# Performance work log

Measured on AMD Instinct MI355X. Metric: run time of the kernel, lower is better.

## Reference

```python
import jax, jax.numpy as jnp
import numpy as np

E, S, G, H, O = 50000, 16, 64, 256, 16


def _mlp(x, W0, b0, W1, b1, W2, b2):
    # x: [..., 2] -> [..., out]
    x = jax.nn.relu(x @ W0 + b0)
    x = jax.nn.relu(x @ W1 + b1)
    return x @ W2 + b2


def setup_inputs() -> dict:
    key = jax.random.key(0)
    ks = jax.random.split(key, 9)
    ob = jax.random.normal(ks[0], (E, S, 3), dtype=jnp.float32)
    action = jax.random.randint(ks[1], (E, S), 0, O).astype(jnp.int64)
    graph_ids = jnp.sort(jax.random.randint(ks[2], (E,), 0, G)).astype(jnp.int32)
    def lin(k, fin, fout):
        return jax.random.normal(k, (fin, fout), dtype=jnp.float32) / jnp.sqrt(jnp.float32(fin))
    return {
        "ob": ob, "action": action, "graph_ids": graph_ids,
        "aW0": lin(ks[3], 2, H), "ab0": jnp.zeros((H,), jnp.float32),
        "aW1": lin(ks[4], H, H), "ab1": jnp.zeros((H,), jnp.float32),
        "aW2": lin(ks[5], H, O), "ab2": jnp.zeros((O,), jnp.float32),
        "cW0": lin(ks[6], 2, H), "cb0": jnp.zeros((H,), jnp.float32),
        "cW1": lin(ks[7], H, H), "cb1": jnp.zeros((H,), jnp.float32),
        "cW2": lin(ks[8], H, 1), "cb2": jnp.zeros((1,), jnp.float32),
    }


def reference(ob, action, graph_ids, aW0, ab0, aW1, ab1, aW2, ab2,
              cW0, cb0, cW1, cb1, cW2, cb2):
    num_edges = ob.shape[0]
    # edge_mask: torch `ob.select(2,0).long() == 0` (truncation toward zero)
    edge_mask = ob[..., 0].astype(jnp.int32) == 0            # [E,S] bool
    mf = edge_mask.astype(ob.dtype)                          # [E,S]
    h = ob[..., 1:3]                                         # [E,S,2]

    # Actor logits over all (edge,sample); mask replaces gather/scatter
    logits = _mlp(h, aW0, ab0, aW1, ab1, aW2, ab2)           # [E,S,O]
    logp = jax.nn.log_softmax(logits, axis=-1)               # [E,S,O]

    # log-prob of given actions, scattered to zeros outside the mask
    alp = jnp.take_along_axis(logp, action[..., None], axis=-1)[..., 0]
    action_log_probs = alp * mf                              # [E,S]

    # critic edge values, scattered to zeros outside the mask
    vals = _mlp(h, cW0, cb0, cW1, cb1, cW2, cb2)[..., 0] * mf  # [E,S]

    # entropy averaged over masked (subgraph) entries only
    ent = -jnp.sum(jnp.exp(logp) * logp, axis=-1)            # [E,S]
    avg_entropy = jnp.sum(ent * mf) / jnp.sum(mf)

    # sum_efeat: per-graph segment sum over edges, divided by num_edges
    value_preds = jax.ops.segment_sum(vals, graph_ids, num_segments=G) / num_edges  # [G,S]

    return action_log_probs, avg_entropy, value_preds, edge_mask
```

## Files before the change

### kernel.cpp

```cpp
#include <hip/hip_runtime.h>
#include <stdint.h>


typedef __attribute__((ext_vector_type(8))) short bf16x8;
typedef __attribute__((ext_vector_type(4))) float f32x4;
typedef __attribute__((ext_vector_type(4))) uint32_t u32x4;

#define NROWS    800000
#define NCHUNK   12500
#define OUT_ENT  800000
#define OUT_VP   800001
#define OUT_MASK 801025

#define SWZ(row) ((((row) & 7) << 4) ^ (((row) & 16) << 1))

__device__ __forceinline__ short f2bf(float x) {
  union { float f; uint32_t u; } v; v.f = x;
  return (short)(uint16_t)((v.u + 0x7FFFu + ((v.u >> 16) & 1u)) >> 16);
}
__device__ __forceinline__ float bf2f(short h) {
  union { uint32_t u; float f; } v; v.u = ((uint32_t)(uint16_t)h) << 16;
  return v.f;
}
template <int C>
__device__ __forceinline__ float dppf(float x) {
  int r = __builtin_amdgcn_update_dpp(0, __builtin_bit_cast(int, x), C, 0xF, 0xF, true);
  return __builtin_bit_cast(float, r);
}
__device__ __forceinline__ float red16_sum(float x) {
  x += dppf<0xB1>(x); x += dppf<0x4E>(x); x += dppf<0x124>(x); x += dppf<0x128>(x); return x;
}
__device__ __forceinline__ float red16_max(float x) {
  x = fmaxf(x, dppf<0xB1>(x)); x = fmaxf(x, dppf<0x4E>(x));
  x = fmaxf(x, dppf<0x124>(x)); x = fmaxf(x, dppf<0x128>(x)); return x;
}
__device__ __forceinline__ uint32_t cvt_pk_bf16(float a, float b) {
  uint32_t r; asm("v_cvt_pk_bf16_f32 %0, %1, %2" : "=v"(r) : "v"(a), "v"(b)); return r;
}

__global__ void zero_kernel(float* out, float* wsf) {
  int t = threadIdx.x + blockIdx.x * blockDim.x;
  for (int i = t; i < 1025; i += 1024) out[OUT_ENT + i] = 0.0f;
  if (t == 0) { wsf[0] = 0.0f; wsf[1] = 0.0f; }
}
__global__ void final_kernel(float* out, const float* wsf) {
  if (threadIdx.x == 0 && blockIdx.x == 0)
    out[OUT_ENT] = (wsf[1] > 0.0f) ? (wsf[0] / wsf[1]) : 0.0f;
}

#define L_ACT1 0
#define L_ACT2 32768
#define L_W2H  65536
#define L_W0   73728
#define L_B0   75776
#define L_OB   76800
#define L_SZ   78848

__global__ void __launch_bounds__(512, 2) ac_main(
    const float* __restrict__ ob, const int* __restrict__ action,
    const int* __restrict__ graph_ids,
    const float* __restrict__ aW0, const float* __restrict__ ab0,
    const float* __restrict__ aW1, const float* __restrict__ ab1,
    const float* __restrict__ aW2, const float* __restrict__ ab2,
    const float* __restrict__ cW0, const float* __restrict__ cb0,
    const float* __restrict__ cW1, const float* __restrict__ cb1,
    const float* __restrict__ cW2, const float* __restrict__ cb2,
    float* __restrict__ out, float* __restrict__ wsf)
{
  extern __shared__ char smem[];
  float* w0buf = (float*)(smem + L_W0);
  float* b0buf = (float*)(smem + L_B0);
  float* obufA = (float*)(smem + L_OB);
  float* vbuf  = (float*)(smem + L_ACT2);
  const f32x4* w04 = (const f32x4*)(smem + L_W0);
  const f32x4* b04 = (const f32x4*)(smem + L_B0);
  __shared__ float went[8], wmf[8];

  const int b = blockIdx.x;
  const int role = (b >> 8) & 1;
  const int pid  = (b & 255) | ((b >> 9) << 8);
  const int stride = 512;

  const int tid = threadIdx.x, lane = tid & 63, wave = tid >> 6;
  const int l15 = lane & 15, l4 = lane >> 4;

  const float* W0s = role ? cW0 : aW0;
  const float* B0s = role ? cb0 : ab0;
  const float* W1s = role ? cW1 : aW1;
  const float* B1s = role ? cb1 : ab1;

  w0buf[tid] = W0s[tid];
  if (tid < 256) b0buf[tid] = B0s[tid];
  if (!role) {
    for (int id = tid; id < 4096; id += 512) {
      int n = id >> 8, k = id & 255;
      *(short*)(smem + L_W2H + n * 512 + ((k * 2) ^ SWZ(n))) = f2bf(aW2[k * 16 + n]);
    }
  }
  const int colbase = wave * 32;
  float b1lane[2] = { B1s[colbase + l15], B1s[colbase + 16 + l15] };
  float b2lane = 0.0f, w2c0 = 0.0f, w2c1 = 0.0f, cb2v = 0.0f;
  if (!role) b2lane = ab2[l15];
  else { w2c0 = cW2[colbase + l15]; w2c1 = cW2[colbase + 16 + l15]; cb2v = cb2[0]; }

  bf16x8 bh[2][8];
  #pragma unroll
  for (int ct = 0; ct < 2; ++ct) {
    const int n = colbase + ct * 16 + l15;
    #pragma unroll
    for (int ks = 0; ks < 8; ++ks) {
      const int k0 = ks * 32 + 8 * l4;
      bf16x8 h8;
      #pragma unroll
      for (int j = 0; j < 8; ++j) h8[j] = f2bf(W1s[(k0 + j) * 256 + n]);
      bh[ct][ks] = h8;
    }
  }
  float sob = 0.0f;
  if (tid < 192) { obufA[tid] = ob[pid * 192 + tid]; }
  { int cn = pid + stride; if (cn < NCHUNK && tid < 192) sob = ob[cn * 192 + tid]; }
  __syncthreads();

  float entacc = 0.0f, mfacc = 0.0f;
  int buf = 0;
  for (int c = pid; c < NCHUNK; c += stride, buf ^= 1) {
    const int row0 = c * 64;
    const float* ocur = obufA + buf * 256;
    float* onxt = (float*)(obufA + (buf ^ 1) * 256);

    if (!role && tid < 64)
      out[OUT_MASK + row0 + tid] = ((int)ocur[tid * 3] == 0) ? 1.0f : 0.0f;
    {
      const int kb = tid & 31;
      f32x4 wa0 = w04[kb * 2], wa1 = w04[kb * 2 + 1];
      f32x4 wb0 = w04[64 + kb * 2], wb1 = w04[64 + kb * 2 + 1];
      f32x4 ba0 = b04[kb * 2], ba1 = b04[kb * 2 + 1];
      #pragma unroll
      for (int i = 0; i < 4; ++i) {
        int row = wave * 2 + 16 * i + (lane >> 5);
        float h0 = ocur[row * 3 + 1], h1 = ocur[row * 3 + 2];
        f32x4 va, vb;
        #pragma unroll
        for (int j = 0; j < 4; ++j) {
          va[j] = fmaxf(fmaf(h0, wa0[j], fmaf(h1, wb0[j], ba0[j])), 0.0f);
          vb[j] = fmaxf(fmaf(h0, wa1[j], fmaf(h1, wb1[j], ba1[j])), 0.0f);
        }
        u32x4 v;
        v[0] = cvt_pk_bf16(va[0], va[1]);
        v[1] = cvt_pk_bf16(va[2], va[3]);
        v[2] = cvt_pk_bf16(vb[0], vb[1]);
        v[3] = cvt_pk_bf16(vb[2], vb[3]);
        *(u32x4*)(smem + L_ACT1 + row * 512 + ((kb * 16) ^ SWZ(row))) = v;
      }
    }
    if (tid < 192) onxt[tid] = sob;
    { int c2 = c + 2 * stride; if (c2 < NCHUNK && tid < 192) sob = ob[c2 * 192 + tid]; }
    __syncthreads();

    float o0w0 = 0.0f;
    if (role && wave == 0) o0w0 = ocur[lane * 3];

    const bool evn = (l15 & 1) == 0;
    #pragma unroll 1
    for (int rtp = 0; rtp < 2; ++rtp) {
      f32x4 acc[2][2];
      #pragma unroll
      for (int h = 0; h < 2; ++h)
        #pragma unroll
        for (int ct = 0; ct < 2; ++ct)
          acc[h][ct] = (f32x4){b1lane[ct], b1lane[ct], b1lane[ct], b1lane[ct]};
      const int rA0 = rtp * 32 + l15, rA1 = rA0 + 16;
      #pragma unroll
      for (int ks = 0; ks < 8; ++ks) {
        const int cb = ks * 64 + 16 * l4;
        bf16x8 a0 = *(const bf16x8*)(smem + L_ACT1 + rA0 * 512 + (cb ^ SWZ(rA0)));
        bf16x8 a1 = *(const bf16x8*)(smem + L_ACT1 + rA1 * 512 + (cb ^ SWZ(rA1)));
        acc[0][0] = __builtin_amdgcn_mfma_f32_16x16x32_bf16(a0, bh[0][ks], acc[0][0], 0, 0, 0);
        acc[0][1] = __builtin_amdgcn_mfma_f32_16x16x32_bf16(a0, bh[1][ks], acc[0][1], 0, 0, 0);
        acc[1][0] = __builtin_amdgcn_mfma_f32_16x16x32_bf16(a1, bh[0][ks], acc[1][0], 0, 0, 0);
        acc[1][1] = __builtin_amdgcn_mfma_f32_16x16x32_bf16(a1, bh[1][ks], acc[1][1], 0, 0, 0);
      }
      if (!role) {
        #pragma unroll
        for (int ct = 0; ct < 2; ++ct) {
          const int colb = (colbase + ct * 16 + (l15 & ~1)) * 2;
          #pragma unroll
          for (int r = 0; r < 4; ++r) {
            float v0 = fmaxf(acc[0][ct][r], 0.0f);
            float v1 = fmaxf(acc[1][ct][r], 0.0f);
            float n0 = dppf<0xB1>(v0), n1 = dppf<0xB1>(v1);
            uint32_t w = cvt_pk_bf16(evn ? v0 : n1, evn ? n0 : v1);
            int rr = rtp * 32 + (evn ? 0 : 16) + 4 * l4 + r;
            *(uint32_t*)(smem + L_ACT2 + rr * 512 + (colb ^ SWZ(rr))) = w;
          }
        }
      } else {
        #pragma unroll
        for (int h = 0; h < 2; ++h) {
          #pragma unroll
          for (int r = 0; r < 4; ++r) {
            float p = fmaxf(acc[h][0][r], 0.0f) * w2c0
                    + fmaxf(acc[h][1][r], 0.0f) * w2c1;
            p = red16_sum(p);
            if (l15 == 0) vbuf[wave * 64 + rtp * 32 + h * 16 + 4 * l4 + r] = p;
          }
        }
      }
    }
    __syncthreads();

    if (!role) {
      const int rt = wave & 3, half = wave >> 2;
      const int rowA = rt * 16 + l15;
      const int swA = SWZ(rowA), swW = SWZ(l15);
      f32x4 ae = {b2lane, b2lane, b2lane, b2lane}, ao = {0.f,0.f,0.f,0.f};
      #pragma unroll
      for (int ks = 0; ks < 8; ks += 2) {
        const int cb0 = ks * 64 + 16 * l4, cb1 = cb0 + 64;
        bf16x8 a0 = *(const bf16x8*)(smem + L_ACT2 + rowA * 512 + (cb0 ^ swA));
        bf16x8 a1 = *(const bf16x8*)(smem + L_ACT2 + rowA * 512 + (cb1 ^ swA));
        bf16x8 w0f = *(const bf16x8*)(smem + L_W2H + l15 * 512 + (cb0 ^ swW));
        bf16x8 w1f = *(const bf16x8*)(smem + L_W2H + l15 * 512 + (cb1 ^ swW));
        ae = __builtin_amdgcn_mfma_f32_16x16x32_bf16(a0, w0f, ae, 0, 0, 0);
        ao = __builtin_amdgcn_mfma_f32_16x16x32_bf16(a1, w1f, ao, 0, 0, 0);
      }
      #pragma unroll
      for (int r2 = 0; r2 < 2; ++r2) {
        const int r = half * 2 + r2;
        const int rl = rt * 16 + 4 * l4 + r;
        float x = ae[r] + ao[r];
        float m = red16_max(x);
        float e = __expf(x - m);
        float s = red16_sum(e);
        float t = red16_sum(e * (x - m));
        float ls = __logf(s);
        float mfr = ((int)ob[(row0 + rl) * 3] == 0) ? 1.0f : 0.0f;
        int av = action[row0 + rl];
        if (l15 == av) out[row0 + rl] = (x - m - ls) * mfr;
        if (l15 == 0) { entacc += (ls - t / s) * mfr; mfacc += mfr; }
      }
    } else {
      if (wave == 0) {
        float v = 0.0f;
        #pragma unroll
        for (int w = 0; w < 8; ++w) v += vbuf[w * 64 + lane];
        if ((int)o0w0 == 0) {
          int g = graph_ids[c * 4 + (lane >> 4)];
          atomicAdd(&out[OUT_VP + g * 16 + (lane & 15)], (v + cb2v) * (1.0f / 50000.0f));
        }
      }
    }
  }
  if (!role) {
    #pragma unroll
    for (int d = 1; d < 64; d <<= 1) { entacc += __shfl_xor(entacc, d); mfacc += __shfl_xor(mfacc, d); }
    if (lane == 0) { went[wave] = entacc; wmf[wave] = mfacc; }
    __syncthreads();
    if (tid == 0) {
      float e = 0.f, m = 0.f;
      #pragma unroll
      for (int i = 0; i < 8; ++i) { e += went[i]; m += wmf[i]; }
      atomicAdd(&wsf[0], e); atomicAdd(&wsf[1], m);
    }
  }
}

extern "C" void kernel_launch(void* const* d_in, const int* in_sizes, int n_in,
                              void* d_out, int out_size, void* d_ws, size_t ws_size,
                              hipStream_t stream) {
  const float* ob     = (const float*)d_in[0];
  const int*   action = (const int*)d_in[1];
  const int*   gids   = (const int*)d_in[2];
  const float* aW0 = (const float*)d_in[3],  *ab0 = (const float*)d_in[4];
  const float* aW1 = (const float*)d_in[5],  *ab1 = (const float*)d_in[6];
  const float* aW2 = (const float*)d_in[7],  *ab2 = (const float*)d_in[8];
  const float* cW0 = (const float*)d_in[9],  *cb0 = (const float*)d_in[10];
  const float* cW1 = (const float*)d_in[11], *cb1 = (const float*)d_in[12];
  const float* cW2 = (const float*)d_in[13], *cb2 = (const float*)d_in[14];
  float* out = (float*)d_out;
  float* wsf = (float*)d_ws;

  zero_kernel<<<2, 512, 0, stream>>>(out, wsf);
  ac_main<<<1024, 512, L_SZ, stream>>>(ob, action, gids, aW0, ab0, aW1, ab1, aW2, ab2,
                                       cW0, cb0, cW1, cb1, cW2, cb2, out, wsf);
  final_kernel<<<1, 64, 0, stream>>>(out, wsf);
}
```

Baseline: 479.5 us.

## Compute layer-0 via MFMA and transpose layer-1 MFMA operands for direct stores

Layer 0 (K=2) is now computed with a bf16 MFMA using register-resident W0 fragments and bias-initialized accumulators, replacing the scalar FMA loop and its LDS weight buffers. The layer-1 MFMA swaps its A/B operands so each lane holds four consecutive columns of one row. That lets ACT2 be written with packed 8-byte stores instead of DPP lane swaps, and lets the critic dot product be reduced with two cross-lane shuffles. Mask values are read from the LDS ob buffer instead of global memory. The layer-0 MFMA wastes most of its K dimension and rounds the inputs h to bf16, a small extra precision loss.

```diff
diff --git a/kernel.cpp b/kernel.cpp
--- a/kernel.cpp
+++ b/kernel.cpp
@@ -4,6 +4,7 @@
 
 typedef __attribute__((ext_vector_type(8))) short bf16x8;
 typedef __attribute__((ext_vector_type(4))) float f32x4;
+typedef __attribute__((ext_vector_type(2))) uint32_t u32x2;
 typedef __attribute__((ext_vector_type(4))) uint32_t u32x4;
 
 #define NROWS    800000
@@ -18,10 +19,6 @@
   union { float f; uint32_t u; } v; v.f = x;
   return (short)(uint16_t)((v.u + 0x7FFFu + ((v.u >> 16) & 1u)) >> 16);
 }
-__device__ __forceinline__ float bf2f(short h) {
-  union { uint32_t u; float f; } v; v.u = ((uint32_t)(uint16_t)h) << 16;
-  return v.f;
-}
 template <int C>
 __device__ __forceinline__ float dppf(float x) {
   int r = __builtin_amdgcn_update_dpp(0, __builtin_bit_cast(int, x), C, 0xF, 0xF, true);
@@ -37,6 +34,9 @@
 __device__ __forceinline__ uint32_t cvt_pk_bf16(float a, float b) {
   uint32_t r; asm("v_cvt_pk_bf16_f32 %0, %1, %2" : "=v"(r) : "v"(a), "v"(b)); return r;
 }
+__device__ __forceinline__ bf16x8 frag_u32(uint32_t a, uint32_t b, uint32_t c, uint32_t d) {
+  union { u32x4 u; bf16x8 h; } v; v.u = (u32x4){a, b, c, d}; return v.h;
+}
 
 __global__ void zero_kernel(float* out, float* wsf) {
   int t = threadIdx.x + blockIdx.x * blockDim.x;
@@ -51,10 +51,8 @@
 #define L_ACT1 0
 #define L_ACT2 32768
 #define L_W2H  65536
-#define L_W0   73728
-#define L_B0   75776
-#define L_OB   76800
-#define L_SZ   78848
+#define L_OB   73728
+#define L_SZ   75776
 
 __global__ void __launch_bounds__(512, 2) ac_main(
     const float* __restrict__ ob, const int* __restrict__ action,
@@ -68,12 +66,8 @@
     float* __restrict__ out, float* __restrict__ wsf)
 {
   extern __shared__ char smem[];
-  float* w0buf = (float*)(smem + L_W0);
-  float* b0buf = (float*)(smem + L_B0);
   float* obufA = (float*)(smem + L_OB);
   float* vbuf  = (float*)(smem + L_ACT2);
-  const f32x4* w04 = (const f32x4*)(smem + L_W0);
-  const f32x4* b04 = (const f32x4*)(smem + L_B0);
   __shared__ float went[8], wmf[8];
 
   const int b = blockIdx.x;
@@ -89,19 +83,34 @@
   const float* W1s = role ? cW1 : aW1;
   const float* B1s = role ? cb1 : ab1;
 
-  w0buf[tid] = W0s[tid];
-  if (tid < 256) b0buf[tid] = B0s[tid];
+  const int colbase = wave * 32;
+
+  bf16x8 w0f[2];
+  #pragma unroll
+  for (int ct = 0; ct < 2; ++ct) {
+    int coln = colbase + ct * 16 + l15;
+    uint32_t p = 0u;
+    if (l4 == 0) p = cvt_pk_bf16(W0s[coln], W0s[256 + coln]);
+    w0f[ct] = frag_u32(p, 0u, 0u, 0u);
+  }
+  f32x4 b0i[2], b1i[2], w2r[2];
+  #pragma unroll
+  for (int ct = 0; ct < 2; ++ct)
+    #pragma unroll
+    for (int r = 0; r < 4; ++r) {
+      int idx = colbase + ct * 16 + 4 * l4 + r;
+      b0i[ct][r] = B0s[idx];
+      b1i[ct][r] = B1s[idx];
+      w2r[ct][r] = role ? cW2[idx] : 0.0f;
+    }
+  float b2lane = 0.0f, cb2v = 0.0f;
   if (!role) {
+    b2lane = ab2[l15];
     for (int id = tid; id < 4096; id += 512) {
       int n = id >> 8, k = id & 255;
       *(short*)(smem + L_W2H + n * 512 + ((k * 2) ^ SWZ(n))) = f2bf(aW2[k * 16 + n]);
     }
-  }
-  const int colbase = wave * 32;
-  float b1lane[2] = { B1s[colbase + l15], B1s[colbase + 16 + l15] };
-  float b2lane = 0.0f, w2c0 = 0.0f, w2c1 = 0.0f, cb2v = 0.0f;
-  if (!role) b2lane = ab2[l15];
-  else { w2c0 = cW2[colbase + l15]; w2c1 = cW2[colbase + 16 + l15]; cb2v = cb2[0]; }
+  } else cb2v = cb2[0];
 
   bf16x8 bh[2][8];
   #pragma unroll
@@ -130,111 +139,109 @@
 
     if (!role && tid < 64)
       out[OUT_MASK + row0 + tid] = ((int)ocur[tid * 3] == 0) ? 1.0f : 0.0f;
-    {
-      const int kb = tid & 31;
-      f32x4 wa0 = w04[kb * 2], wa1 = w04[kb * 2 + 1];
-      f32x4 wb0 = w04[64 + kb * 2], wb1 = w04[64 + kb * 2 + 1];
-      f32x4 ba0 = b04[kb * 2], ba1 = b04[kb * 2 + 1];
-      #pragma unroll
-      for (int i = 0; i < 4; ++i) {
-        int row = wave * 2 + 16 * i + (lane >> 5);
-        float h0 = ocur[row * 3 + 1], h1 = ocur[row * 3 + 2];
-        f32x4 va, vb;
-        #pragma unroll
-        for (int j = 0; j < 4; ++j) {
-          va[j] = fmaxf(fmaf(h0, wa0[j], fmaf(h1, wb0[j], ba0[j])), 0.0f);
-          vb[j] = fmaxf(fmaf(h0, wa1[j], fmaf(h1, wb1[j], ba1[j])), 0.0f);
-        }
-        u32x4 v;
-        v[0] = cvt_pk_bf16(va[0], va[1]);
-        v[1] = cvt_pk_bf16(va[2], va[3]);
-        v[2] = cvt_pk_bf16(vb[0], vb[1]);
-        v[3] = cvt_pk_bf16(vb[2], vb[3]);
-        *(u32x4*)(smem + L_ACT1 + row * 512 + ((kb * 16) ^ SWZ(row))) = v;
+    #pragma unroll
+    for (int rt = 0; rt < 4; ++rt) {
+      const int rowr = rt * 16 + l15;
+      float h0 = ocur[rowr * 3 + 1], h1 = ocur[rowr * 3 + 2];
+      uint32_t hp = (l4 == 0) ? cvt_pk_bf16(h0, h1) : 0u;
+      bf16x8 hf = frag_u32(hp, 0u, 0u, 0u);
+      #pragma unroll
+      for (int ct = 0; ct < 2; ++ct) {
+        f32x4 a = __builtin_amdgcn_mfma_f32_16x16x32_bf16(w0f[ct], hf, b0i[ct], 0, 0, 0);
+        u32x2 w;
+        w[0] = cvt_pk_bf16(fmaxf(a[0], 0.0f), fmaxf(a[1], 0.0f));
+        w[1] = cvt_pk_bf16(fmaxf(a[2], 0.0f), fmaxf(a[3], 0.0f));
+        *(u32x2*)(smem + L_ACT1 + rowr * 512 +
+                  ((colbase * 2 + ct * 32 + 8 * l4) ^ SWZ(rowr))) = w;
       }
     }
     if (tid < 192) onxt[tid] = sob;
     { int c2 = c + 2 * stride; if (c2 < NCHUNK && tid < 192) sob = ob[c2 * 192 + tid]; }
     __syncthreads();
 
-    float o0w0 = 0.0f;
-    if (role && wave == 0) o0w0 = ocur[lane * 3];
-
-    const bool evn = (l15 & 1) == 0;
     #pragma unroll 1
     for (int rtp = 0; rtp < 2; ++rtp) {
       f32x4 acc[2][2];
       #pragma unroll
-      for (int h = 0; h < 2; ++h)
-        #pragma unroll
-        for (int ct = 0; ct < 2; ++ct)
-          acc[h][ct] = (f32x4){b1lane[ct], b1lane[ct], b1lane[ct], b1lane[ct]};
-      const int rA0 = rtp * 32 + l15, rA1 = rA0 + 16;
+      for (int rt = 0; rt < 2; ++rt)
+        #pragma unroll
+        for (int ct = 0; ct < 2; ++ct) acc[rt][ct] = b1i[ct];
+      const int rB0 = rtp * 32 + l15, rB1 = rB0 + 16;
       #pragma unroll
       for (int ks = 0; ks < 8; ++ks) {
         const int cb = ks * 64 + 16 * l4;
-        bf16x8 a0 = *(const bf16x8*)(smem + L_ACT1 + rA0 * 512 + (cb ^ SWZ(rA0)));
-        bf16x8 a1 = *(const bf16x8*)(smem + L_ACT1 + rA1 * 512 + (cb ^ SWZ(rA1)));
-        acc[0][0] = __builtin_amdgcn_mfma_f32_16x16x32_bf16(a0, bh[0][ks], acc[0][0], 0, 0, 0);
-        acc[0][1] = __builtin_amdgcn_mfma_f32_16x16x32_bf16(a0, bh[1][ks], acc[0][1], 0, 0, 0);
-        acc[1][0] = __builtin_amdgcn_mfma_f32_16x16x32_bf16(a1, bh[0][ks], acc[1][0], 0, 0, 0);
-        acc[1][1] = __builtin_amdgcn_mfma_f32_16x16x32_bf16(a1, bh[1][ks], acc[1][1], 0, 0, 0);
+        bf16x8 a0 = *(const bf16x8*)(smem + L_ACT1 + rB0 * 512 + (cb ^ SWZ(rB0)));
+        bf16x8 a1 = *(const bf16x8*)(smem + L_ACT1 + rB1 * 512 + (cb ^ SWZ(rB1)));
+        acc[0][0] = __builtin_amdgcn_mfma_f32_16x16x32_bf16(bh[0][ks], a0, acc[0][0], 0, 0, 0);
+        acc[0][1] = __builtin_amdgcn_mfma_f32_16x16x32_bf16(bh[1][ks], a0, acc[0][1], 0, 0, 0);
+        acc[1][0] = __builtin_amdgcn_mfma_f32_16x16x32_bf16(bh[0][ks], a1, acc[1][0], 0, 0, 0);
+        acc[1][1] = __builtin_amdgcn_mfma_f32_16x16x32_bf16(bh[1][ks], a1, acc[1][1], 0, 0, 0);
       }
       if (!role) {
         #pragma unroll
-        for (int ct = 0; ct < 2; ++ct) {
-          const int colb = (colbase + ct * 16 + (l15 & ~1)) * 2;
+        for (int rt = 0; rt < 2; ++rt) {
+          const int row = rtp * 32 + rt * 16 + l15;
+          const int sw = SWZ(row);
           #pragma unroll
-          for (int r = 0; r < 4; ++r) {
-            float v0 = fmaxf(acc[0][ct][r], 0.0f);
-            float v1 = fmaxf(acc[1][ct][r], 0.0f);
-            float n0 = dppf<0xB1>(v0), n1 = dppf<0xB1>(v1);
-            uint32_t w = cvt_pk_bf16(evn ? v0 : n1, evn ? n0 : v1);
-            int rr = rtp * 32 + (evn ? 0 : 16) + 4 * l4 + r;
-            *(uint32_t*)(smem + L_ACT2 + rr * 512 + (colb ^ SWZ(rr))) = w;
+          for (int ct = 0; ct < 2; ++ct) {
+            u32x2 w;
+            w[0] = cvt_pk_bf16(fmaxf(acc[rt][ct][0], 0.0f), fmaxf(acc[rt][ct][1], 0.0f));
+            w[1] = cvt_pk_bf16(fmaxf(acc[rt][ct][2], 0.0f), fmaxf(acc[rt][ct][3], 0.0f));
+            *(u32x2*)(smem + L_ACT2 + row * 512 +
+                      ((colbase * 2 + ct * 32 + 8 * l4) ^ sw)) = w;
           }
         }
       } else {
         #pragma unroll
-        for (int h = 0; h < 2; ++h) {
+        for (int rt = 0; rt < 2; ++rt) {
+          float p = 0.0f;
           #pragma unroll
-          for (int r = 0; r < 4; ++r) {
-            float p = fmaxf(acc[h][0][r], 0.0f) * w2c0
-                    + fmaxf(acc[h][1][r], 0.0f) * w2c1;
-            p = red16_sum(p);
-            if (l15 == 0) vbuf[wave * 64 + rtp * 32 + h * 16 + 4 * l4 + r] = p;
-          }
+          for (int ct = 0; ct < 2; ++ct)
+            #pragma unroll
+            for (int r = 0; r < 4; ++r)
+              p = fmaf(fmaxf(acc[rt][ct][r], 0.0f), w2r[ct][r], p);
+          p += __shfl_xor(p, 16);
+          p += __shfl_xor(p, 32);
+          if (l4 == 0) vbuf[wave * 64 + rtp * 32 + rt * 16 + l15] = p;
         }
       }
     }
+    float mk0 = 0.0f, mk1 = 0.0f, o0w0 = 0.0f;
+    if (!role) {
+      const int rt4 = wave & 3, hf2 = wave >> 2;
+      const int rl0 = rt4 * 16 + 4 * l4 + hf2 * 2;
+      mk0 = ocur[rl0 * 3];
+      mk1 = ocur[(rl0 + 1) * 3];
+    } else if (wave == 0) o0w0 = ocur[lane * 3];
     __syncthreads();
 
     if (!role) {
-      const int rt = wave & 3, half = wave >> 2;
-      const int rowA = rt * 16 + l15;
+      const int rt4 = wave & 3, hf2 = wave >> 2;
+      const int rowA = rt4 * 16 + l15;
       const int swA = SWZ(rowA), swW = SWZ(l15);
-      f32x4 ae = {b2lane, b2lane, b2lane, b2lane}, ao = {0.f,0.f,0.f,0.f};
+      f32x4 ae = {b2lane, b2lane, b2lane, b2lane}, ao = {0.f, 0.f, 0.f, 0.f};
       #pragma unroll
       for (int ks = 0; ks < 8; ks += 2) {
         const int cb0 = ks * 64 + 16 * l4, cb1 = cb0 + 64;
         bf16x8 a0 = *(const bf16x8*)(smem + L_ACT2 + rowA * 512 + (cb0 ^ swA));
         bf16x8 a1 = *(const bf16x8*)(smem + L_ACT2 + rowA * 512 + (cb1 ^ swA));
-        bf16x8 w0f = *(const bf16x8*)(smem + L_W2H + l15 * 512 + (cb0 ^ swW));
-        bf16x8 w1f = *(const bf16x8*)(smem + L_W2H + l15 * 512 + (cb1 ^ swW));
-        ae = __builtin_amdgcn_mfma_f32_16x16x32_bf16(a0, w0f, ae, 0, 0, 0);
-        ao = __builtin_amdgcn_mfma_f32_16x16x32_bf16(a1, w1f, ao, 0, 0, 0);
-      }
+        bf16x8 w0h = *(const bf16x8*)(smem + L_W2H + l15 * 512 + (cb0 ^ swW));
+        bf16x8 w1h = *(const bf16x8*)(smem + L_W2H + l15 * 512 + (cb1 ^ swW));
+        ae = __builtin_amdgcn_mfma_f32_16x16x32_bf16(a0, w0h, ae, 0, 0, 0);
+        ao = __builtin_amdgcn_mfma_f32_16x16x32_bf16(a1, w1h, ao, 0, 0, 0);
+      }
+      float mks[2] = { mk0, mk1 };
       #pragma unroll
       for (int r2 = 0; r2 < 2; ++r2) {
-        const int r = half * 2 + r2;
-        const int rl = rt * 16 + 4 * l4 + r;
+        const int r = hf2 * 2 + r2;
+        const int rl = rt4 * 16 + 4 * l4 + r;
         float x = ae[r] + ao[r];
         float m = red16_max(x);
         float e = __expf(x - m);
         float s = red16_sum(e);
         float t = red16_sum(e * (x - m));
         float ls = __logf(s);
-        float mfr = ((int)ob[(row0 + rl) * 3] == 0) ? 1.0f : 0.0f;
+        float mfr = ((int)mks[r2] == 0) ? 1.0f : 0.0f;
         int av = action[row0 + rl];
         if (l15 == av) out[row0 + rl] = (x - m - ls) * mfr;
         if (l15 == 0) { entacc += (ls - t / s) * mfr; mfacc += mfr; }
```

After: 456.1 us. 1.05x faster.
